# Optimization experiments

Measured on AMD Instinct MI355X. Metric: run time of the kernel, lower is better.

## Reference

```python
import jax, jax.numpy as jnp
import numpy as np

H = 8          # num_heads
T = 2          # num_edge_types
NEG_SLOPE = 0.2


def _edge_softmax(scores, dst, num_nodes):
    # softmax over incoming edges of each destination node, per head
    m = jax.ops.segment_max(scores, dst, num_segments=num_nodes)  # [N,H]
    e = jnp.exp(scores - m[dst])                                   # [E,H]
    s = jax.ops.segment_sum(e, dst, num_segments=num_nodes)        # [N,H]
    return e / s[dst]


def setup_inputs() -> dict:
    key = jax.random.key(0)
    ks = jax.random.split(key, 8)
    N, D, E = 50000, 128, 800000
    return {
        "x": jax.random.normal(ks[0], (N, D), dtype=jnp.float32),
        "w_u": jax.random.normal(ks[1], (H * T, D), dtype=jnp.float32) * (1.0 / np.sqrt(D)),
        "b_u": jax.random.normal(ks[2], (H * T,), dtype=jnp.float32) * 0.01,
        "w_v": jax.random.normal(ks[3], (H * T, D), dtype=jnp.float32) * (1.0 / np.sqrt(D)),
        "src_e0": jax.random.randint(ks[4], (E,), 0, N, dtype=jnp.int32),
        "dst_e0": jax.random.randint(ks[5], (E,), 0, N, dtype=jnp.int32),
        "src_e1": jax.random.randint(ks[6], (E,), 0, N, dtype=jnp.int32),
        "dst_e1": jax.random.randint(ks[7], (E,), 0, N, dtype=jnp.int32),
    }


def reference(x, w_u, b_u, w_v, src_e0, dst_e0, src_e1, dst_e1):
    N, D = x.shape
    head_dim = D // H
    scores_u = x @ w_u.T + b_u   # [N, H*T]
    scores_v = x @ w_v.T         # [N, H*T]
    xh = x.reshape(N, head_dim, H)  # matches torch reshape(-1, head_dim, num_heads)
    outs = [x]  # sep=True
    for t, (src, dst) in enumerate([(src_e0, dst_e0), (src_e1, dst_e1)]):
        u = scores_u[:, t * H:(t + 1) * H]
        v = scores_v[:, t * H:(t + 1) * H]
        s = u[src] + v[dst]                         # u_add_v -> [E,H]
        s = jnp.where(s >= 0, s, NEG_SLOPE * s)     # LeakyReLU(0.2)
        p = _edge_softmax(s, dst, N)                # [E,H]
        msg = xh[src] * p[:, None, :]               # u_mul_e -> [E,head_dim,H]
        agg = jax.ops.segment_sum(msg, dst, num_segments=N)  # [N,head_dim,H]
        outs.append(agg.reshape(N, D))
    return jnp.concatenate(outs, axis=-1)  # [N, D*(1+T)]
```

## Files before the change

kernel.cpp:

```cpp
#include <hip/hip_runtime.h>

#define NEG_SLOPE 0.2f
#define RSHIFT 6
#define RW     64
#define MAXNR  800
#define CHUNKP 8192

__device__ __forceinline__ ushort f2bf(float f) {
    union { float f; unsigned u; } c; c.f = f;
    unsigned u = c.u;
    return (ushort)((u + 0x7fffu + ((u >> 16) & 1u)) >> 16);
}

__global__ __launch_bounds__(256) void mega_kernel(
    const float* __restrict__ x, const float* __restrict__ wu,
    const float* __restrict__ bu, const float* __restrict__ wv,
    const int* __restrict__ s0, const int* __restrict__ d0,
    const int* __restrict__ s1, const int* __restrict__ d1,
    float* __restrict__ out, ushort* __restrict__ xbf,
    float* __restrict__ su, float* __restrict__ sv,
    int* __restrict__ gcur, unsigned* __restrict__ pairs,
    int N, int E, int nr, int cap, int convBlocks, int scoreBlocks, int ppset)
{
    __shared__ float wlds[32 * 129];
    int* smi = (int*)wlds;
    int tid = threadIdx.x;
    int bid = blockIdx.x;

    if (bid < convBlocks) {
        int i = bid * 256 + tid;
        if (i < N * 32) {
            float4 v = ((const float4*)x)[i];
            int n = i >> 5, q = i & 31;
            ((float4*)out)[(size_t)n * 96 + q] = v;
            ushort4 b;
            b.x = f2bf(v.x); b.y = f2bf(v.y); b.z = f2bf(v.z); b.w = f2bf(v.w);
            *(ushort4*)(xbf + (size_t)i * 4) = b;
        }
        return;
    }
    if (bid < convBlocks + scoreBlocks) {
        for (int i = tid; i < 4096; i += 256) {
            int o = i >> 7, k = i & 127;
            wlds[o * 129 + k] = (o < 16) ? wu[i] : wv[i - 2048];
        }
        __syncthreads();
        int o = tid & 15;
        int n = (bid - convBlocks) * 16 + (tid >> 4);
        if (n >= N) return;
        const float4* xr4 = (const float4*)(x + (size_t)n * 128);
        const float* wur = wlds + o * 129;
        const float* wvr = wlds + (16 + o) * 129;
        float au = 0.f, av = 0.f;
#pragma unroll
        for (int kk = 0; kk < 32; ++kk) {
            float4 xv = xr4[kk];
            int k = kk * 4;
            au = fmaf(xv.x, wur[k],     au);  av = fmaf(xv.x, wvr[k],     av);
            au = fmaf(xv.y, wur[k + 1], au);  av = fmaf(xv.y, wvr[k + 1], av);
            au = fmaf(xv.z, wur[k + 2], au);  av = fmaf(xv.z, wvr[k + 2], av);
            au = fmaf(xv.w, wur[k + 3], au);  av = fmaf(xv.w, wvr[k + 3], av);
        }
        su[n * 16 + o] = au + bu[o];
        sv[n * 16 + o] = av;
        return;
    }
    int pb = bid - convBlocks - scoreBlocks;
    int t = pb / ppset, c = pb % ppset;
    const int* ss = t ? s1 : s0;
    const int* dd = t ? d1 : d0;
    int beg = c * CHUNKP, end = min(E, beg + CHUNKP);
    int* lcnt = smi; int* gb = smi + MAXNR; int* lrun = smi + 2 * MAXNR;
    for (int i = tid; i < nr; i += 256) lcnt[i] = 0;
    __syncthreads();
    for (int e = beg + tid; e < end; e += 256)
        atomicAdd(&lcnt[dd[e] >> RSHIFT], 1);
    __syncthreads();
    for (int i = tid; i < nr; i += 256) {
        gb[i] = atomicAdd(&gcur[t * nr + i], lcnt[i]);
        lrun[i] = 0;
    }
    __syncthreads();
    unsigned* pt = pairs + (size_t)t * nr * cap;
    for (int e = beg + tid; e < end; e += 256) {
        int dst = dd[e], src = ss[e];
        int r = dst >> RSHIFT;
        int pos = atomicAdd(&lrun[r], 1);
        pt[(size_t)r * cap + gb[r] + pos] = ((unsigned)dst << 16) | (unsigned)src;
    }
}

__global__ __launch_bounds__(256, 8) void buildagg_kernel(
    const ushort* __restrict__ xbf, const float* __restrict__ su,
    const float* __restrict__ sv, const int* __restrict__ gcur,
    const unsigned* __restrict__ pairs, float* __restrict__ out,
    int N, int E, int nr, int cap)
{
    __shared__ ushort srcs[1408];
    __shared__ int offl[65];
    __shared__ int cursor[64];
    __shared__ __align__(16) float ev4[4][512];
    int r = blockIdx.x, t = blockIdx.y, tid = threadIdx.x;
    int m = gcur[t * nr + r];
    if (m > cap) m = cap;
    const unsigned* p = pairs + ((size_t)t * nr + r) * cap;

    if (tid < 64) cursor[tid] = 0;
    __syncthreads();
    for (int i = tid; i < m; i += 256)
        atomicAdd(&cursor[(p[i] >> 16) & (RW - 1)], 1);
    __syncthreads();
    if (tid < 64) {
        int v = cursor[tid];
        int incl = v;
#pragma unroll
        for (int d = 1; d < 64; d <<= 1) {
            int o = __shfl(incl, tid - d);
            if (tid >= d) incl += o;
        }
        offl[tid + 1] = incl;
        if (tid == 0) offl[0] = 0;
        cursor[tid] = incl - v;
    }
    __syncthreads();
    for (int i = tid; i < m; i += 256) {
        unsigned v = p[i];
        int pos = atomicAdd(&cursor[(v >> 16) & (RW - 1)], 1);
        srcs[pos] = (ushort)(v & 0xffffu);
    }
    __syncthreads();

    int wid = tid >> 6, lane = tid & 63;
    int h = lane & 7, e8 = lane >> 3;
    int hf = lane >> 5, q = lane & 31;
    int j0 = q * 4, hbase = (q & 1) * 4;
    float* ev = ev4[wid];
    for (int ln = wid; ln < RW; ln += 4) {
        int n = (r << RSHIFT) + ln;
        if (n >= N) break;
        int beg = offl[ln], end = offl[ln + 1];
        float vh = sv[n * 16 + t * 8 + h];
        float acc0 = 0.f, acc1 = 0.f, acc2 = 0.f, acc3 = 0.f;
        float l = 0.f;
        for (int cbeg = beg; cbeg < end; cbeg += 64) {
            int cnt = min(end - cbeg, 64);
            int gmax = (cnt + 7) >> 3;
            for (int g = 0; g < gmax; ++g) {
                int e = g * 8 + e8;
                bool valid = e < cnt;
                int srcv = srcs[cbeg + (valid ? e : 0)];
                float sc = su[srcv * 16 + t * 8 + h] + vh;
                sc = (sc >= 0.f) ? sc : NEG_SLOPE * sc;
                float ee = valid ? __expf(sc) : 0.f;
                l += ee;
                ev[e * 8 + h] = ee;
            }
            int pairs2 = (cnt + 1) >> 1;
            for (int i2 = 0; i2 < pairs2; ++i2) {
                int eidx = i2 * 2 + hf;
                int srcv = srcs[cbeg + ((eidx < cnt) ? eidx : 0)];
                float4 p4 = *(const float4*)(ev + eidx * 8 + hbase);
                uint2 u = *(const uint2*)(xbf + (size_t)srcv * 128 + j0);
                float x0 = __uint_as_float(u.x << 16);
                float x1 = __uint_as_float(u.x & 0xffff0000u);
                float x2 = __uint_as_float(u.y << 16);
                float x3 = __uint_as_float(u.y & 0xffff0000u);
                acc0 = fmaf(x0, p4.x, acc0);
                acc1 = fmaf(x1, p4.y, acc1);
                acc2 = fmaf(x2, p4.z, acc2);
                acc3 = fmaf(x3, p4.w, acc3);
            }
        }
        l += __shfl_xor(l, 8);
        l += __shfl_xor(l, 16);
        l += __shfl_xor(l, 32);
        float invl = (l > 0.f) ? (1.f / l) : 0.f;
        acc0 += __shfl_xor(acc0, 32);
        acc1 += __shfl_xor(acc1, 32);
        acc2 += __shfl_xor(acc2, 32);
        acc3 += __shfl_xor(acc3, 32);
        float i0 = __shfl(invl, hbase);
        float i1 = __shfl(invl, hbase + 1);
        float i2v = __shfl(invl, hbase + 2);
        float i3 = __shfl(invl, hbase + 3);
        if (hf == 0) {
            float4 r4 = make_float4(acc0 * i0, acc1 * i1, acc2 * i2v, acc3 * i3);
            *(float4*)(out + (size_t)n * 384 + 128 + (size_t)t * 128 + j0) = r4;
        }
    }
}

extern "C" void kernel_launch(void* const* d_in, const int* in_sizes, int n_in,
                              void* d_out, int out_size, void* d_ws, size_t ws_size,
                              hipStream_t stream)
{
    const float* x  = (const float*)d_in[0];
    const float* wu = (const float*)d_in[1];
    const float* bu = (const float*)d_in[2];
    const float* wv = (const float*)d_in[3];
    const int* s0 = (const int*)d_in[4];
    const int* d0 = (const int*)d_in[5];
    const int* s1 = (const int*)d_in[6];
    const int* d1 = (const int*)d_in[7];
    float* out = (float*)d_out;
    int N = in_sizes[0] / 128;
    int E = in_sizes[4];

    int nr = ((N - 1) >> RSHIFT) + 1;
    long long mean = (long long)RW * E / N;
    int cap = (int)(mean + mean / 4 + 64);

    char* ws = (char*)d_ws;
    size_t o = 0;
    auto alloc = [&](size_t bytes) -> void* {
        void* p = ws + o;
        o = (o + bytes + 255) & ~(size_t)255;
        return p;
    };
    float* su       = (float*)alloc((size_t)N * 16 * 4);
    float* sv       = (float*)alloc((size_t)N * 16 * 4);
    int* gcur       = (int*)alloc((size_t)2 * nr * 4);
    unsigned* pairs = (unsigned*)alloc((size_t)2 * nr * cap * 4);
    ushort* xbf     = (ushort*)alloc((size_t)N * 128 * 2);

    int convBlocks  = (N * 32 + 255) / 256;
    int scoreBlocks = (N + 15) / 16;
    int ppset       = (E + CHUNKP - 1) / CHUNKP;

    hipMemsetAsync(gcur, 0, (size_t)2 * nr * 4, stream);
    mega_kernel<<<convBlocks + scoreBlocks + 2 * ppset, 256, 0, stream>>>(
        x, wu, bu, wv, s0, d0, s1, d1, out, xbf, su, sv,
        gcur, pairs, N, E, nr, cap, convBlocks, scoreBlocks, ppset);
    buildagg_kernel<<<dim3(nr, 2), 256, 0, stream>>>(
        xbf, su, sv, gcur, pairs, out, N, E, nr, cap);
}
```

Baseline: 261.8 us.

## Reorder mega-kernel roles, register-block score GEMV, widen gather to 8 features

The fused preprocessing kernel now schedules the edge-partition blocks first, so the atomic-heavy, long-running work starts earliest. The conversion blocks each handle 8 float4 elements instead of 1. The score projection gives each thread 4 nodes, reusing the LDS weight loads across nodes. In the aggregation kernel, each lane now gathers 8 bf16 features (uint4) over 4 edges per step instead of 4 features over 2 edges, with extra cross-lane reductions at the end. The aim is fewer, wider memory transactions and better latency hiding, at the cost of more registers and a costlier final shuffle reduction.

```diff
diff --git a/kernel.cpp b/kernel.cpp
--- a/kernel.cpp
+++ b/kernel.cpp
@@ -20,15 +20,90 @@
     float* __restrict__ out, ushort* __restrict__ xbf,
     float* __restrict__ su, float* __restrict__ sv,
     int* __restrict__ gcur, unsigned* __restrict__ pairs,
-    int N, int E, int nr, int cap, int convBlocks, int scoreBlocks, int ppset)
+    int N, int E, int nr, int cap, int partBlocks, int scoreBlocks, int ppset)
 {
     __shared__ float wlds[32 * 129];
     int* smi = (int*)wlds;
     int tid = threadIdx.x;
     int bid = blockIdx.x;
 
-    if (bid < convBlocks) {
-        int i = bid * 256 + tid;
+    if (bid < partBlocks) {
+        int t = bid / ppset, c = bid % ppset;
+        const int* ss = t ? s1 : s0;
+        const int* dd = t ? d1 : d0;
+        int beg = c * CHUNKP, end = min(E, beg + CHUNKP);
+        int* lcnt = smi; int* gb = smi + MAXNR; int* lrun = smi + 2 * MAXNR;
+        for (int i = tid; i < nr; i += 256) lcnt[i] = 0;
+        __syncthreads();
+        for (int e = beg + tid; e < end; e += 256)
+            atomicAdd(&lcnt[dd[e] >> RSHIFT], 1);
+        __syncthreads();
+        for (int i = tid; i < nr; i += 256) {
+            gb[i] = atomicAdd(&gcur[t * nr + i], lcnt[i]);
+            lrun[i] = 0;
+        }
+        __syncthreads();
+        unsigned* pt = pairs + (size_t)t * nr * cap;
+        for (int e = beg + tid; e < end; e += 256) {
+            int dst = dd[e], src = ss[e];
+            int r = dst >> RSHIFT;
+            int pos = atomicAdd(&lrun[r], 1);
+            pt[(size_t)r * cap + gb[r] + pos] = ((unsigned)dst << 16) | (unsigned)src;
+        }
+        return;
+    }
+    if (bid < partBlocks + scoreBlocks) {
+        for (int i = tid; i < 4096; i += 256) {
+            int o = i >> 7, k = i & 127;
+            wlds[o * 129 + k] = (o < 16) ? wu[i] : wv[i - 2048];
+        }
+        __syncthreads();
+        int o = tid & 15, slot = tid >> 4;
+        int n0 = (bid - partBlocks) * 64 + slot * 4;
+        int na = min(n0,     N - 1), nb2 = min(n0 + 1, N - 1);
+        int nc = min(n0 + 2, N - 1), nd = min(n0 + 3, N - 1);
+        const float4* xa = (const float4*)(x + (size_t)na * 128);
+        const float4* xb = (const float4*)(x + (size_t)nb2 * 128);
+        const float4* xc = (const float4*)(x + (size_t)nc * 128);
+        const float4* xd = (const float4*)(x + (size_t)nd * 128);
+        const float* wur = wlds + o * 129;
+        const float* wvr = wlds + (16 + o) * 129;
+        float au0 = 0.f, au1 = 0.f, au2 = 0.f, au3 = 0.f;
+        float av0 = 0.f, av1 = 0.f, av2 = 0.f, av3 = 0.f;
+#pragma unroll
+        for (int kk = 0; kk < 32; ++kk) {
+            int k = kk * 4;
+            float wu0 = wur[k], wu1 = wur[k + 1], wu2 = wur[k + 2], wu3 = wur[k + 3];
+            float wv0 = wvr[k], wv1 = wvr[k + 1], wv2 = wvr[k + 2], wv3 = wvr[k + 3];
+            float4 a = xa[kk], b = xb[kk], cc = xc[kk], dd4 = xd[kk];
+            au0 = fmaf(a.x, wu0, au0);  av0 = fmaf(a.x, wv0, av0);
+            au0 = fmaf(a.y, wu1, au0);  av0 = fmaf(a.y, wv1, av0);
+            au0 = fmaf(a.z, wu2, au0);  av0 = fmaf(a.z, wv2, av0);
+            au0 = fmaf(a.w, wu3, au0);  av0 = fmaf(a.w, wv3, av0);
+            au1 = fmaf(b.x, wu0, au1);  av1 = fmaf(b.x, wv0, av1);
+            au1 = fmaf(b.y, wu1, au1);  av1 = fmaf(b.y, wv1, av1);
+            au1 = fmaf(b.z, wu2, au1);  av1 = fmaf(b.z, wv2, av1);
+            au1 = fmaf(b.w, wu3, au1);  av1 = fmaf(b.w, wv3, av1);
+            au2 = fmaf(cc.x, wu0, au2); av2 = fmaf(cc.x, wv0, av2);
+            au2 = fmaf(cc.y, wu1, au2); av2 = fmaf(cc.y, wv1, av2);
+            au2 = fmaf(cc.z, wu2, au2); av2 = fmaf(cc.z, wv2, av2);
+            au2 = fmaf(cc.w, wu3, au2); av2 = fmaf(cc.w, wv3, av2);
+            au3 = fmaf(dd4.x, wu0, au3); av3 = fmaf(dd4.x, wv0, av3);
+            au3 = fmaf(dd4.y, wu1, au3); av3 = fmaf(dd4.y, wv1, av3);
+            au3 = fmaf(dd4.z, wu2, au3); av3 = fmaf(dd4.z, wv2, av3);
+            au3 = fmaf(dd4.w, wu3, au3); av3 = fmaf(dd4.w, wv3, av3);
+        }
+        float bo = bu[o];
+        if (n0 < N)     { su[n0 * 16 + o]       = au0 + bo; sv[n0 * 16 + o]       = av0; }
+        if (n0 + 1 < N) { su[(n0 + 1) * 16 + o] = au1 + bo; sv[(n0 + 1) * 16 + o] = av1; }
+        if (n0 + 2 < N) { su[(n0 + 2) * 16 + o] = au2 + bo; sv[(n0 + 2) * 16 + o] = av2; }
+        if (n0 + 3 < N) { su[(n0 + 3) * 16 + o] = au3 + bo; sv[(n0 + 3) * 16 + o] = av3; }
+        return;
+    }
+    int base = (bid - partBlocks - scoreBlocks) * 2048 + tid;
+#pragma unroll
+    for (int j = 0; j < 8; ++j) {
+        int i = base + j * 256;
         if (i < N * 32) {
             float4 v = ((const float4*)x)[i];
             int n = i >> 5, q = i & 31;
@@ -37,56 +112,6 @@
             b.x = f2bf(v.x); b.y = f2bf(v.y); b.z = f2bf(v.z); b.w = f2bf(v.w);
             *(ushort4*)(xbf + (size_t)i * 4) = b;
         }
-        return;
-    }
-    if (bid < convBlocks + scoreBlocks) {
-        for (int i = tid; i < 4096; i += 256) {
-            int o = i >> 7, k = i & 127;
-            wlds[o * 129 + k] = (o < 16) ? wu[i] : wv[i - 2048];
-        }
-        __syncthreads();
-        int o = tid & 15;
-        int n = (bid - convBlocks) * 16 + (tid >> 4);
-        if (n >= N) return;
-        const float4* xr4 = (const float4*)(x + (size_t)n * 128);
-        const float* wur = wlds + o * 129;
-        const float* wvr = wlds + (16 + o) * 129;
-        float au = 0.f, av = 0.f;
-#pragma unroll
-        for (int kk = 0; kk < 32; ++kk) {
-            float4 xv = xr4[kk];
-            int k = kk * 4;
-            au = fmaf(xv.x, wur[k],     au);  av = fmaf(xv.x, wvr[k],     av);
-            au = fmaf(xv.y, wur[k + 1], au);  av = fmaf(xv.y, wvr[k + 1], av);
-            au = fmaf(xv.z, wur[k + 2], au);  av = fmaf(xv.z, wvr[k + 2], av);
-            au = fmaf(xv.w, wur[k + 3], au);  av = fmaf(xv.w, wvr[k + 3], av);
-        }
-        su[n * 16 + o] = au + bu[o];
-        sv[n * 16 + o] = av;
-        return;
-    }
-    int pb = bid - convBlocks - scoreBlocks;
-    int t = pb / ppset, c = pb % ppset;
-    const int* ss = t ? s1 : s0;
-    const int* dd = t ? d1 : d0;
-    int beg = c * CHUNKP, end = min(E, beg + CHUNKP);
-    int* lcnt = smi; int* gb = smi + MAXNR; int* lrun = smi + 2 * MAXNR;
-    for (int i = tid; i < nr; i += 256) lcnt[i] = 0;
-    __syncthreads();
-    for (int e = beg + tid; e < end; e += 256)
-        atomicAdd(&lcnt[dd[e] >> RSHIFT], 1);
-    __syncthreads();
-    for (int i = tid; i < nr; i += 256) {
-        gb[i] = atomicAdd(&gcur[t * nr + i], lcnt[i]);
-        lrun[i] = 0;
-    }
-    __syncthreads();
-    unsigned* pt = pairs + (size_t)t * nr * cap;
-    for (int e = beg + tid; e < end; e += 256) {
-        int dst = dd[e], src = ss[e];
-        int r = dst >> RSHIFT;
-        int pos = atomicAdd(&lrun[r], 1);
-        pt[(size_t)r * cap + gb[r] + pos] = ((unsigned)dst << 16) | (unsigned)src;
     }
 }
 
@@ -132,15 +157,16 @@
 
     int wid = tid >> 6, lane = tid & 63;
     int h = lane & 7, e8 = lane >> 3;
-    int hf = lane >> 5, q = lane & 31;
-    int j0 = q * 4, hbase = (q & 1) * 4;
+    int qtr = lane >> 4, q16 = lane & 15;
+    int j0 = q16 * 8;
     float* ev = ev4[wid];
     for (int ln = wid; ln < RW; ln += 4) {
         int n = (r << RSHIFT) + ln;
         if (n >= N) break;
         int beg = offl[ln], end = offl[ln + 1];
         float vh = sv[n * 16 + t * 8 + h];
-        float acc0 = 0.f, acc1 = 0.f, acc2 = 0.f, acc3 = 0.f;
+        float a0 = 0.f, a1 = 0.f, a2 = 0.f, a3 = 0.f;
+        float a4 = 0.f, a5 = 0.f, a6 = 0.f, a7 = 0.f;
         float l = 0.f;
         for (int cbeg = beg; cbeg < end; cbeg += 64) {
             int cnt = min(end - cbeg, 64);
@@ -155,37 +181,44 @@
                 l += ee;
                 ev[e * 8 + h] = ee;
             }
-            int pairs2 = (cnt + 1) >> 1;
-            for (int i2 = 0; i2 < pairs2; ++i2) {
-                int eidx = i2 * 2 + hf;
+            int quads = (cnt + 3) >> 2;
+#pragma unroll 2
+            for (int i4 = 0; i4 < quads; ++i4) {
+                int eidx = i4 * 4 + qtr;
                 int srcv = srcs[cbeg + ((eidx < cnt) ? eidx : 0)];
-                float4 p4 = *(const float4*)(ev + eidx * 8 + hbase);
-                uint2 u = *(const uint2*)(xbf + (size_t)srcv * 128 + j0);
-                float x0 = __uint_as_float(u.x << 16);
-                float x1 = __uint_as_float(u.x & 0xffff0000u);
-                float x2 = __uint_as_float(u.y << 16);
-                float x3 = __uint_as_float(u.y & 0xffff0000u);
-                acc0 = fmaf(x0, p4.x, acc0);
-                acc1 = fmaf(x1, p4.y, acc1);
-                acc2 = fmaf(x2, p4.z, acc2);
-                acc3 = fmaf(x3, p4.w, acc3);
+                float4 pa = *(const float4*)(ev + eidx * 8);
+                float4 pb = *(const float4*)(ev + eidx * 8 + 4);
+                uint4 u = *(const uint4*)(xbf + (size_t)srcv * 128 + j0);
+                a0 = fmaf(__uint_as_float(u.x << 16),          pa.x, a0);
+                a1 = fmaf(__uint_as_float(u.x & 0xffff0000u),  pa.y, a1);
+                a2 = fmaf(__uint_as_float(u.y << 16),          pa.z, a2);
+                a3 = fmaf(__uint_as_float(u.y & 0xffff0000u),  pa.w, a3);
+                a4 = fmaf(__uint_as_float(u.z << 16),          pb.x, a4);
+                a5 = fmaf(__uint_as_float(u.z & 0xffff0000u),  pb.y, a5);
+                a6 = fmaf(__uint_as_float(u.w << 16),          pb.z, a6);
+                a7 = fmaf(__uint_as_float(u.w & 0xffff0000u),  pb.w, a7);
             }
         }
         l += __shfl_xor(l, 8);
         l += __shfl_xor(l, 16);
         l += __shfl_xor(l, 32);
         float invl = (l > 0.f) ? (1.f / l) : 0.f;
-        acc0 += __shfl_xor(acc0, 32);
-        acc1 += __shfl_xor(acc1, 32);
-        acc2 += __shfl_xor(acc2, 32);
-        acc3 += __shfl_xor(acc3, 32);
-        float i0 = __shfl(invl, hbase);
-        float i1 = __shfl(invl, hbase + 1);
-        float i2v = __shfl(invl, hbase + 2);
-        float i3 = __shfl(invl, hbase + 3);
-        if (hf == 0) {
-            float4 r4 = make_float4(acc0 * i0, acc1 * i1, acc2 * i2v, acc3 * i3);
-            *(float4*)(out + (size_t)n * 384 + 128 + (size_t)t * 128 + j0) = r4;
+        a0 += __shfl_xor(a0, 16); a0 += __shfl_xor(a0, 32);
+        a1 += __shfl_xor(a1, 16); a1 += __shfl_xor(a1, 32);
+        a2 += __shfl_xor(a2, 16); a2 += __shfl_xor(a2, 32);
+        a3 += __shfl_xor(a3, 16); a3 += __shfl_xor(a3, 32);
+        a4 += __shfl_xor(a4, 16); a4 += __shfl_xor(a4, 32);
+        a5 += __shfl_xor(a5, 16); a5 += __shfl_xor(a5, 32);
+        a6 += __shfl_xor(a6, 16); a6 += __shfl_xor(a6, 32);
+        a7 += __shfl_xor(a7, 16); a7 += __shfl_xor(a7, 32);
+        float i0 = __shfl(invl, 0), i1 = __shfl(invl, 1);
+        float i2 = __shfl(invl, 2), i3 = __shfl(invl, 3);
+        float i4v = __shfl(invl, 4), i5 = __shfl(invl, 5);
+        float i6 = __shfl(invl, 6), i7 = __shfl(invl, 7);
+        if (qtr == 0) {
+            float* orow = out + (size_t)n * 384 + 128 + (size_t)t * 128 + j0;
+            *(float4*)orow       = make_float4(a0 * i0, a1 * i1, a2 * i2, a3 * i3);
+            *(float4*)(orow + 4) = make_float4(a4 * i4v, a5 * i5, a6 * i6, a7 * i7);
         }
     }
 }
@@ -223,14 +256,15 @@
     unsigned* pairs = (unsigned*)alloc((size_t)2 * nr * cap * 4);
     ushort* xbf     = (ushort*)alloc((size_t)N * 128 * 2);
 
-    int convBlocks  = (N * 32 + 255) / 256;
-    int scoreBlocks = (N + 15) / 16;
     int ppset       = (E + CHUNKP - 1) / CHUNKP;
+    int partBlocks  = 2 * ppset;
+    int scoreBlocks = (N + 63) / 64;
+    int convBlocks  = (N * 32 + 2047) / 2048;
 
     hipMemsetAsync(gcur, 0, (size_t)2 * nr * 4, stream);
-    mega_kernel<<<convBlocks + scoreBlocks + 2 * ppset, 256, 0, stream>>>(
+    mega_kernel<<<partBlocks + scoreBlocks + convBlocks, 256, 0, stream>>>(
         x, wu, bu, wv, s0, d0, s1, d1, out, xbf, su, sv,
-        gcur, pairs, N, E, nr, cap, convBlocks, scoreBlocks, ppset);
+        gcur, pairs, N, E, nr, cap, partBlocks, scoreBlocks, ppset);
     buildagg_kernel<<<dim3(nr, 2), 256, 0, stream>>>(
         xbf, su, sv, gcur, pairs, out, N, E, nr, cap);
 }
```

Result: slower. 336.5 us (+28.6%).
